# Kernel optimization log

Hardware: AMD Instinct MI355X
Metric: run time of the kernel (lower is better)

The kernel has to match this reference:

```python
import jax, jax.numpy as jnp
import numpy as np

IN_SHAPE = (8, 16, 8)     # hidden_shape, prod = 1024
FF_SHAPE = (16, 16, 16)   # ff_shape, prod = 4096
RANKS = (1, 8, 8, 1)      # tt_ranks


def _make_cores(key, in_shape, out_shape, ranks):
    cores = []
    for k in range(3):
        key, sub = jax.random.split(key)
        shape = (ranks[k], in_shape[k], out_shape[k], ranks[k + 1])
        # glorot-ish scale per core
        scale = (2.0 / (in_shape[k] * ranks[k] + out_shape[k] * ranks[k + 1])) ** 0.5
        cores.append(jax.random.normal(sub, shape, dtype=jnp.float32) * scale)
    return key, cores


def setup_inputs() -> dict:
    key = jax.random.key(0)
    key, kx = jax.random.split(key)
    x = jax.random.normal(kx, (8192, int(np.prod(IN_SHAPE))), dtype=jnp.float32)
    key, c0 = _make_cores(key, IN_SHAPE, FF_SHAPE, RANKS)
    key, c1 = _make_cores(key, FF_SHAPE, IN_SHAPE, RANKS)
    b0 = jnp.zeros((int(np.prod(FF_SHAPE)),), dtype=jnp.float32)
    b1 = jnp.zeros((int(np.prod(IN_SHAPE)),), dtype=jnp.float32)
    return {
        "x": x,
        "c0a": c0[0], "c0b": c0[1], "c0c": c0[2], "b0": b0,
        "c1a": c1[0], "c1b": c1[1], "c1c": c1[2], "b1": b1,
    }


def tt_linear(x, cores, bias, in_shape, out_shape):
    # x: (B, prod(in_shape)); cores[k]: (r_k, in_k, out_k, r_{k+1})
    B = x.shape[0]
    t = x.reshape(B, *in_shape)                      # (B, i, j, k)
    t = jnp.einsum('bijk,aior->bjkor', t, cores[0])  # (B, j, k, o1, r1)
    t = jnp.einsum('bjkor,rjps->bkops', t, cores[1]) # (B, k, o1, o2, r2)
    t = jnp.einsum('bkops,skqu->bopq', t, cores[2])  # (B, o1, o2, o3)
    return t.reshape(B, -1) + bias


def reference(x, c0a, c0b, c0c, b0, c1a, c1b, c1c, b1):
    h = tt_linear(x, (c0a, c0b, c0c), b0, IN_SHAPE, FF_SHAPE)
    h = jax.nn.gelu(h, approximate=False)  # nn.GELU default = exact erf form
    out = tt_linear(h, (c1a, c1b, c1c), b1, FF_SHAPE, IN_SHAPE)
    return out
```

## Files before the change

kernel.cpp:

```cpp
#include <hip/hip_runtime.h>
#include <math.h>

typedef _Float16 f16x8 __attribute__((ext_vector_type(8)));
typedef _Float16 f16x4 __attribute__((ext_vector_type(4)));
typedef float f32x16 __attribute__((ext_vector_type(16)));

__device__ __forceinline__ void async_copy16(const void* g, void* l) {
    __builtin_amdgcn_global_load_lds(
        (const __attribute__((address_space(1))) void*)g,
        (__attribute__((address_space(3))) void*)l, 16, 0, 0);
}

__global__ __launch_bounds__(256) void prep_kernel(
    const float* __restrict__ x, _Float16* __restrict__ xh,
    const float* __restrict__ c0a, const float* __restrict__ c0b,
    const float* __restrict__ c0c, _Float16* __restrict__ W0t,
    const float* __restrict__ c1a, const float* __restrict__ c1b,
    const float* __restrict__ c1c, _Float16* __restrict__ W1t) {
    __shared__ float G[16384];
    const int b = blockIdx.x, t = threadIdx.x;
    if (b < 1024) {
        const float4* in4 = (const float4*)x;
        f16x4* out4 = (f16x4*)xh;
        const int base = b * 2048 + t;
#pragma unroll
        for (int u = 0; u < 8; ++u) {
            float4 v = in4[base + u * 256];
            f16x4 o;
            o[0] = (_Float16)v.x; o[1] = (_Float16)v.y;
            o[2] = (_Float16)v.z; o[3] = (_Float16)v.w;
            out4[base + u * 256] = o;
        }
    } else if (b < 1280) {
        const int o = (b - 1024) >> 4, p = (b - 1024) & 15;
#pragma unroll
        for (int n = 0; n < 64; ++n) {
            int idx = t + 256 * n;
            int k = idx & 7, j = (idx >> 3) & 15, r = (idx >> 7) & 7, q = idx >> 10;
            float s = 0.f;
#pragma unroll
            for (int ss = 0; ss < 8; ++ss)
                s += c0b[((r * 16 + j) * 16 + p) * 8 + ss] * c0c[(ss * 8 + k) * 16 + q];
            G[idx] = s;
        }
        __syncthreads();
        const int i = t >> 5, j = (t >> 1) & 15, kq = t & 1;
        float a[8];
#pragma unroll
        for (int r = 0; r < 8; ++r) a[r] = c0a[(i * 16 + o) * 8 + r];
        const float4* G4 = (const float4*)G;
#pragma unroll
        for (int q = 0; q < 16; ++q) {
            float4 acc = {0.f, 0.f, 0.f, 0.f};
#pragma unroll
            for (int r = 0; r < 8; ++r) {
                float4 g = G4[q * 256 + r * 32 + j * 2 + kq];
                acc.x += a[r] * g.x; acc.y += a[r] * g.y;
                acc.z += a[r] * g.z; acc.w += a[r] * g.w;
            }
            f16x4 h4;
            h4[0] = (_Float16)acc.x; h4[1] = (_Float16)acc.y;
            h4[2] = (_Float16)acc.z; h4[3] = (_Float16)acc.w;
            *(f16x4*)(W0t + (size_t)((o * 16 + p) * 16 + q) * 1024 + t * 4) = h4;
        }
    } else {
        const int o = (b - 1280) >> 4, p = (b - 1280) & 15;
#pragma unroll
        for (int n = 0; n < 64; ++n) {
            int idx = t + 256 * n;
            int k = idx & 15, j = (idx >> 4) & 15, r = (idx >> 8) & 7, q = idx >> 11;
            float s = 0.f;
#pragma unroll
            for (int ss = 0; ss < 8; ++ss)
                s += c1b[((r * 16 + j) * 16 + p) * 8 + ss] * c1c[(ss * 16 + k) * 8 + q];
            G[idx] = s;
        }
        __syncthreads();
        const int ig = t >> 6, j = (t >> 2) & 15, kq = t & 3;
        float a[4][8];
#pragma unroll
        for (int ii = 0; ii < 4; ++ii)
#pragma unroll
            for (int r = 0; r < 8; ++r) a[ii][r] = c1a[((ig * 4 + ii) * 8 + o) * 8 + r];
        const float4* G4 = (const float4*)G;
#pragma unroll
        for (int q = 0; q < 8; ++q) {
            float4 acc[4] = {{0,0,0,0},{0,0,0,0},{0,0,0,0},{0,0,0,0}};
#pragma unroll
            for (int r = 0; r < 8; ++r) {
                float4 g = G4[q * 512 + r * 64 + j * 4 + kq];
#pragma unroll
                for (int ii = 0; ii < 4; ++ii) {
                    acc[ii].x += a[ii][r] * g.x; acc[ii].y += a[ii][r] * g.y;
                    acc[ii].z += a[ii][r] * g.z; acc[ii].w += a[ii][r] * g.w;
                }
            }
            const size_t rowbase = (size_t)((o * 16 + p) * 8 + q) * 4096;
#pragma unroll
            for (int ii = 0; ii < 4; ++ii) {
                f16x4 h4;
                h4[0] = (_Float16)acc[ii].x; h4[1] = (_Float16)acc[ii].y;
                h4[2] = (_Float16)acc[ii].z; h4[3] = (_Float16)acc[ii].w;
                *(f16x4*)(W1t + rowbase + (ig * 4 + ii) * 256 + j * 16 + kq * 4) = h4;
            }
        }
    }
}

template <int OUTMODE>
__global__ __launch_bounds__(256) void gemm32_kernel(
    const _Float16* __restrict__ A, const _Float16* __restrict__ Bt,
    const float* __restrict__ bias, void* __restrict__ Cout,
    int M, int N, int K) {
    constexpr int BK = 64;
    __shared__ alignas(16) _Float16 sA[128 * BK];
    __shared__ alignas(16) _Float16 sB[128 * BK];

    const int t = threadIdx.x, lane = t & 63, w = t >> 6;
    const int m0 = blockIdx.x * 128, n0 = blockIdx.y * 128;
    const int wm = (w & 1) * 64, wn = (w >> 1) * 64;
    const int l31 = lane & 31, lh = lane >> 5;
    const int fl = (l31 & 7) ^ (2 * (l31 >> 3));

    f32x16 acc[2][2] = {};

    const int s0 = w * 256 + lane;
    const int row0 = s0 >> 3;
    const int kof0 = ((lane & 7) ^ (lane >> 3)) * 8;
    const _Float16* gA = A + (size_t)(m0 + row0) * K;
    const _Float16* gB = Bt + (size_t)(n0 + row0) * K;
    _Float16* lA = sA + s0 * 8;
    _Float16* lB = sB + s0 * 8;
    const size_t rs = (size_t)8 * K;

    for (int k0 = 0; k0 < K; k0 += BK) {
#pragma unroll
        for (int m = 0; m < 4; ++m) {
            const int ko = k0 + (kof0 ^ (16 * m));
            async_copy16(gA + m * rs + ko, lA + m * 512);
            async_copy16(gB + m * rs + ko, lB + m * 512);
        }
        __syncthreads();
#pragma unroll
        for (int kk = 0; kk < 4; ++kk) {
            f16x8 af[2], bf[2];
            const int sl = ((kk * 2 + lh) ^ fl) * 8;
#pragma unroll
            for (int i = 0; i < 2; ++i) {
                af[i] = *(const f16x8*)(sA + (wm + i * 32 + l31) * BK + sl);
                bf[i] = *(const f16x8*)(sB + (wn + i * 32 + l31) * BK + sl);
            }
#pragma unroll
            for (int i = 0; i < 2; ++i)
#pragma unroll
                for (int j = 0; j < 2; ++j)
                    acc[i][j] = __builtin_amdgcn_mfma_f32_32x32x16_f16(af[i], bf[j], acc[i][j], 0, 0, 0);
        }
        __syncthreads();
    }

#pragma unroll
    for (int i = 0; i < 2; ++i)
#pragma unroll
        for (int j = 0; j < 2; ++j) {
            const int col = n0 + wn + j * 32 + l31;
            const float bv = bias[col];
            const int rbase = m0 + wm + i * 32 + 4 * lh;
            if (OUTMODE == 1) {
                _Float16* C = (_Float16*)Cout;
#pragma unroll
                for (int r = 0; r < 16; ++r) {
                    int row = rbase + (r & 3) + 8 * (r >> 2);
                    float v = acc[i][j][r] + bv;
                    float uu = v * (0.7978845608028654f + 0.0356774081363001f * v * v);
                    float e = __builtin_amdgcn_exp2f(uu * 2.8853900817779268f);
                    float rc = __builtin_amdgcn_rcpf(e + 1.0f);
                    C[(size_t)row * N + col] = (_Float16)(v * (1.0f - rc));
                }
            } else {
                float* C = (float*)Cout;
#pragma unroll
                for (int r = 0; r < 16; ++r) {
                    int row = rbase + (r & 3) + 8 * (r >> 2);
                    C[(size_t)row * N + col] = acc[i][j][r] + bv;
                }
            }
        }
}

extern "C" void kernel_launch(void* const* d_in, const int* in_sizes, int n_in,
                              void* d_out, int out_size, void* d_ws, size_t ws_size,
                              hipStream_t stream) {
    const float* x   = (const float*)d_in[0];
    const float* c0a = (const float*)d_in[1];
    const float* c0b = (const float*)d_in[2];
    const float* c0c = (const float*)d_in[3];
    const float* b0  = (const float*)d_in[4];
    const float* c1a = (const float*)d_in[5];
    const float* c1b = (const float*)d_in[6];
    const float* c1c = (const float*)d_in[7];
    const float* b1  = (const float*)d_in[8];
    float* out = (float*)d_out;

    char* ws = (char*)d_ws;
    _Float16* xh  = (_Float16*)(ws);
    _Float16* W0t = (_Float16*)(ws + (size_t)(16u << 20));
    _Float16* W1t = (_Float16*)(ws + (size_t)(24u << 20));
    _Float16* h   = (_Float16*)(ws + (size_t)(32u << 20));

    prep_kernel<<<dim3(1408), dim3(256), 0, stream>>>(
        x, xh, c0a, c0b, c0c, W0t, c1a, c1b, c1c, W1t);
    gemm32_kernel<1><<<dim3(64, 32), dim3(256), 0, stream>>>(
        xh, W0t, b0, (void*)h, 8192, 4096, 1024);
    gemm32_kernel<0><<<dim3(64, 8), dim3(256), 0, stream>>>(
        h, W1t, b1, (void*)out, 8192, 1024, 4096);
}
```

Before: 307.4 us.

## Double-buffer GEMM LDS tiles and switch to k-plane-major LDS layout

Both GEMM kernels now keep two LDS stages per operand and issue async global-to-LDS loads for the next K tile before computing on the current one, with a single barrier per iteration. This is meant to hide global load latency behind MFMA work. The LDS layout also changes from an XOR-swizzled row-major tile to k-chunk planes, where each lane copies contiguous 16-byte segments per row. LDS use doubles to 64KB per block, which may lower occupancy. The new layout could also change bank-conflict behaviour and global coalescing.

Result: slower. 448.4 us (+45.9%).

```diff
diff --git a/kernel.cpp b/kernel.cpp
--- a/kernel.cpp
+++ b/kernel.cpp
@@ -108,47 +108,50 @@
 }
 
 template <int OUTMODE>
-__global__ __launch_bounds__(256) void gemm32_kernel(
+__global__ __launch_bounds__(256) void gemm32db_kernel(
     const _Float16* __restrict__ A, const _Float16* __restrict__ Bt,
     const float* __restrict__ bias, void* __restrict__ Cout,
     int M, int N, int K) {
-    constexpr int BK = 64;
-    __shared__ alignas(16) _Float16 sA[128 * BK];
-    __shared__ alignas(16) _Float16 sB[128 * BK];
+    __shared__ alignas(16) _Float16 sA[2][8192];
+    __shared__ alignas(16) _Float16 sB[2][8192];
 
     const int t = threadIdx.x, lane = t & 63, w = t >> 6;
     const int m0 = blockIdx.x * 128, n0 = blockIdx.y * 128;
     const int wm = (w & 1) * 64, wn = (w >> 1) * 64;
     const int l31 = lane & 31, lh = lane >> 5;
-    const int fl = (l31 & 7) ^ (2 * (l31 >> 3));
 
     f32x16 acc[2][2] = {};
 
-    const int s0 = w * 256 + lane;
-    const int row0 = s0 >> 3;
-    const int kof0 = ((lane & 7) ^ (lane >> 3)) * 8;
-    const _Float16* gA = A + (size_t)(m0 + row0) * K;
-    const _Float16* gB = Bt + (size_t)(n0 + row0) * K;
-    _Float16* lA = sA + s0 * 8;
-    _Float16* lB = sB + s0 * 8;
-    const size_t rs = (size_t)8 * K;
-
-    for (int k0 = 0; k0 < K; k0 += BK) {
-#pragma unroll
-        for (int m = 0; m < 4; ++m) {
-            const int ko = k0 + (kof0 ^ (16 * m));
-            async_copy16(gA + m * rs + ko, lA + m * 512);
-            async_copy16(gB + m * rs + ko, lB + m * 512);
-        }
+    const _Float16* gA = A + (size_t)(m0 + (w & 1) * 64 + lane) * K + (w >> 1) * 8;
+    const _Float16* gB = Bt + (size_t)(n0 + (w & 1) * 64 + lane) * K + (w >> 1) * 8;
+    const int ldst = w * 512 + lane * 8;
+
+    const int nit = K >> 6;
+#pragma unroll
+    for (int m = 0; m < 4; ++m) {
+        async_copy16(gA + m * 16, &sA[0][ldst + m * 2048]);
+        async_copy16(gB + m * 16, &sB[0][ldst + m * 2048]);
+    }
+
+    for (int it = 0; it < nit; ++it) {
         __syncthreads();
+        const int cur = it & 1;
+        if (it + 1 < nit) {
+            const int k0 = (it + 1) << 6;
+#pragma unroll
+            for (int m = 0; m < 4; ++m) {
+                async_copy16(gA + k0 + m * 16, &sA[cur ^ 1][ldst + m * 2048]);
+                async_copy16(gB + k0 + m * 16, &sB[cur ^ 1][ldst + m * 2048]);
+            }
+        }
 #pragma unroll
         for (int kk = 0; kk < 4; ++kk) {
             f16x8 af[2], bf[2];
-            const int sl = ((kk * 2 + lh) ^ fl) * 8;
+            const int pl = (2 * kk + lh) * 1024;
 #pragma unroll
             for (int i = 0; i < 2; ++i) {
-                af[i] = *(const f16x8*)(sA + (wm + i * 32 + l31) * BK + sl);
-                bf[i] = *(const f16x8*)(sB + (wn + i * 32 + l31) * BK + sl);
+                af[i] = *(const f16x8*)(&sA[cur][pl + (wm + i * 32 + l31) * 8]);
+                bf[i] = *(const f16x8*)(&sB[cur][pl + (wn + i * 32 + l31) * 8]);
             }
 #pragma unroll
             for (int i = 0; i < 2; ++i)
@@ -156,7 +159,6 @@
                 for (int j = 0; j < 2; ++j)
                     acc[i][j] = __builtin_amdgcn_mfma_f32_32x32x16_f16(af[i], bf[j], acc[i][j], 0, 0, 0);
         }
-        __syncthreads();
     }
 
 #pragma unroll
@@ -210,8 +212,8 @@
 
     prep_kernel<<<dim3(1408), dim3(256), 0, stream>>>(
         x, xh, c0a, c0b, c0c, W0t, c1a, c1b, c1c, W1t);
-    gemm32_kernel<1><<<dim3(64, 32), dim3(256), 0, stream>>>(
+    gemm32db_kernel<1><<<dim3(64, 32), dim3(256), 0, stream>>>(
         xh, W0t, b0, (void*)h, 8192, 4096, 1024);
-    gemm32_kernel<0><<<dim3(64, 8), dim3(256), 0, stream>>>(
+    gemm32db_kernel<0><<<dim3(64, 8), dim3(256), 0, stream>>>(
         h, W1t, b1, (void*)out, 8192, 1024, 4096);
 }
```

## Split-K the second GEMM into two halves with an fp16 partial and reduce kernel

Applied to the files above, without the earlier changes.

The second GEMM (K=4096, only 512 tiles) is split along K into two z-slices, doubling the block count to fill more CUs. Slice 0 writes fp32 output plus bias, and slice 1 writes an fp16 partial into the workspace, reusing the xh buffer. A separate reduce kernel then adds the partial into the output. This adds an extra launch and extra memory traffic, and rounding the partial sum to fp16 loses some precision.

Result: slower. 320.3 us (+4.2%).

```diff
diff --git a/kernel.cpp b/kernel.cpp
--- a/kernel.cpp
+++ b/kernel.cpp
@@ -107,10 +107,9 @@
     }
 }
 
-template <int OUTMODE>
-__global__ __launch_bounds__(256) void gemm32_kernel(
+__global__ __launch_bounds__(256) void gemm32_g1_kernel(
     const _Float16* __restrict__ A, const _Float16* __restrict__ Bt,
-    const float* __restrict__ bias, void* __restrict__ Cout,
+    const float* __restrict__ bias, _Float16* __restrict__ C,
     int M, int N, int K) {
     constexpr int BK = 64;
     __shared__ alignas(16) _Float16 sA[128 * BK];
@@ -147,8 +146,8 @@
             const int sl = ((kk * 2 + lh) ^ fl) * 8;
 #pragma unroll
             for (int i = 0; i < 2; ++i) {
-                af[i] = *(const f16x8*)(sA + (wm + i * 32 + l31) * BK + sl);
-                bf[i] = *(const f16x8*)(sB + (wn + i * 32 + l31) * BK + sl);
+                af[i] = *(const f16x8*)(&sA[(wm + i * 32 + l31) * 64 + sl]);
+                bf[i] = *(const f16x8*)(&sB[(wn + i * 32 + l31) * 64 + sl]);
             }
 #pragma unroll
             for (int i = 0; i < 2; ++i)
@@ -166,26 +165,108 @@
             const int col = n0 + wn + j * 32 + l31;
             const float bv = bias[col];
             const int rbase = m0 + wm + i * 32 + 4 * lh;
-            if (OUTMODE == 1) {
-                _Float16* C = (_Float16*)Cout;
+#pragma unroll
+            for (int r = 0; r < 16; ++r) {
+                int row = rbase + (r & 3) + 8 * (r >> 2);
+                float v = acc[i][j][r] + bv;
+                float uu = v * (0.7978845608028654f + 0.0356774081363001f * v * v);
+                float e = __builtin_amdgcn_exp2f(uu * 2.8853900817779268f);
+                float rc = __builtin_amdgcn_rcpf(e + 1.0f);
+                C[(size_t)row * N + col] = (_Float16)(v * (1.0f - rc));
+            }
+        }
+}
+
+__global__ __launch_bounds__(256) void gemm32_g2s_kernel(
+    const _Float16* __restrict__ A, const _Float16* __restrict__ Bt,
+    const float* __restrict__ bias, float* __restrict__ C0,
+    _Float16* __restrict__ C1, int M, int N, int K, int klen) {
+    constexpr int BK = 64;
+    __shared__ alignas(16) _Float16 sA[128 * BK];
+    __shared__ alignas(16) _Float16 sB[128 * BK];
+
+    const int t = threadIdx.x, lane = t & 63, w = t >> 6;
+    const int m0 = blockIdx.x * 128, n0 = blockIdx.y * 128;
+    const int kbeg = blockIdx.z * klen;
+    const int wm = (w & 1) * 64, wn = (w >> 1) * 64;
+    const int l31 = lane & 31, lh = lane >> 5;
+    const int fl = (l31 & 7) ^ (2 * (l31 >> 3));
+
+    f32x16 acc[2][2] = {};
+
+    const int s0 = w * 256 + lane;
+    const int row0 = s0 >> 3;
+    const int kof0 = ((lane & 7) ^ (lane >> 3)) * 8;
+    const _Float16* gA = A + (size_t)(m0 + row0) * K + kbeg;
+    const _Float16* gB = Bt + (size_t)(n0 + row0) * K + kbeg;
+    _Float16* lA = sA + s0 * 8;
+    _Float16* lB = sB + s0 * 8;
+    const size_t rs = (size_t)8 * K;
+
+    for (int k0 = 0; k0 < klen; k0 += BK) {
+#pragma unroll
+        for (int m = 0; m < 4; ++m) {
+            const int ko = k0 + (kof0 ^ (16 * m));
+            async_copy16(gA + m * rs + ko, lA + m * 512);
+            async_copy16(gB + m * rs + ko, lB + m * 512);
+        }
+        __syncthreads();
+#pragma unroll
+        for (int kk = 0; kk < 4; ++kk) {
+            f16x8 af[2], bf[2];
+            const int sl = ((kk * 2 + lh) ^ fl) * 8;
+#pragma unroll
+            for (int i = 0; i < 2; ++i) {
+                af[i] = *(const f16x8*)(&sA[(wm + i * 32 + l31) * 64 + sl]);
+                bf[i] = *(const f16x8*)(&sB[(wn + i * 32 + l31) * 64 + sl]);
+            }
+#pragma unroll
+            for (int i = 0; i < 2; ++i)
+#pragma unroll
+                for (int j = 0; j < 2; ++j)
+                    acc[i][j] = __builtin_amdgcn_mfma_f32_32x32x16_f16(af[i], bf[j], acc[i][j], 0, 0, 0);
+        }
+        __syncthreads();
+    }
+
+    if (blockIdx.z == 0) {
+#pragma unroll
+        for (int i = 0; i < 2; ++i)
+#pragma unroll
+            for (int j = 0; j < 2; ++j) {
+                const int col = n0 + wn + j * 32 + l31;
+                const float bv = bias[col];
+                const int rbase = m0 + wm + i * 32 + 4 * lh;
 #pragma unroll
                 for (int r = 0; r < 16; ++r) {
                     int row = rbase + (r & 3) + 8 * (r >> 2);
-                    float v = acc[i][j][r] + bv;
-                    float uu = v * (0.7978845608028654f + 0.0356774081363001f * v * v);
-                    float e = __builtin_amdgcn_exp2f(uu * 2.8853900817779268f);
-                    float rc = __builtin_amdgcn_rcpf(e + 1.0f);
-                    C[(size_t)row * N + col] = (_Float16)(v * (1.0f - rc));
+                    C0[(size_t)row * N + col] = acc[i][j][r] + bv;
                 }
-            } else {
-                float* C = (float*)Cout;
+            }
+    } else {
+#pragma unroll
+        for (int i = 0; i < 2; ++i)
+#pragma unroll
+            for (int j = 0; j < 2; ++j) {
+                const int col = n0 + wn + j * 32 + l31;
+                const int rbase = m0 + wm + i * 32 + 4 * lh;
 #pragma unroll
                 for (int r = 0; r < 16; ++r) {
                     int row = rbase + (r & 3) + 8 * (r >> 2);
-                    C[(size_t)row * N + col] = acc[i][j][r] + bv;
+                    C1[(size_t)row * N + col] = (_Float16)acc[i][j][r];
                 }
             }
-        }
+    }
+}
+
+__global__ __launch_bounds__(256) void reduce_add_kernel(
+    float4* __restrict__ out, const f16x4* __restrict__ p1) {
+    int i = blockIdx.x * 256 + threadIdx.x;
+    float4 o = out[i];
+    f16x4 p = p1[i];
+    o.x += (float)p[0]; o.y += (float)p[1];
+    o.z += (float)p[2]; o.w += (float)p[3];
+    out[i] = o;
 }
 
 extern "C" void kernel_launch(void* const* d_in, const int* in_sizes, int n_in,
@@ -207,11 +288,13 @@
     _Float16* W0t = (_Float16*)(ws + (size_t)(16u << 20));
     _Float16* W1t = (_Float16*)(ws + (size_t)(24u << 20));
     _Float16* h   = (_Float16*)(ws + (size_t)(32u << 20));
+    _Float16* p1  = (_Float16*)(ws);
 
     prep_kernel<<<dim3(1408), dim3(256), 0, stream>>>(
         x, xh, c0a, c0b, c0c, W0t, c1a, c1b, c1c, W1t);
-    gemm32_kernel<1><<<dim3(64, 32), dim3(256), 0, stream>>>(
-        xh, W0t, b0, (void*)h, 8192, 4096, 1024);
-    gemm32_kernel<0><<<dim3(64, 8), dim3(256), 0, stream>>>(
-        h, W1t, b1, (void*)out, 8192, 1024, 4096);
-}
+    gemm32_g1_kernel<<<dim3(64, 32), dim3(256), 0, stream>>>(
+        xh, W0t, b0, h, 8192, 4096, 1024);
+    gemm32_g2s_kernel<<<dim3(64, 8, 2), dim3(256), 0, stream>>>(
+        h, W1t, b1, out, p1, 8192, 1024, 4096, 2048);
+    reduce_add_kernel<<<dim3(8192), dim3(256), 0, stream>>>((float4*)out, (const f16x4*)p1);
+}
```
